# Kernel optimization log

Measured on AMD Instinct MI355X. Metric: run time of the kernel, lower is better.

## Reference

```python
import jax, jax.numpy as jnp
import numpy as np

FS = 20.832e6      # sampling rate [Hz]
FDEMOD = 5.208e6   # demodulation frequency [Hz]
C = 1540.0         # sound speed [m/s]
FNUM = 1.0
MIN_W = 1e-3
EPS = 1e-5         # BatchNorm eps
EVENT = 0
TWO_PI = 2.0 * np.pi


def _cba(x, w, b, g, beta, pad):
    # Conv2d (NCHW) + BatchNorm2d (training-mode batch stats, biased var) + ReLU
    y = jax.lax.conv_general_dilated(x, w, (1, 1), ((0, 0), (pad, pad)),
                                     dimension_numbers=('NCHW', 'OIHW', 'NCHW'))
    y = y + b[None, :, None, None]
    mu = jnp.mean(y, axis=(0, 2, 3), keepdims=True)
    var = jnp.mean((y - mu) ** 2, axis=(0, 2, 3), keepdims=True)
    y = (y - mu) * jax.lax.rsqrt(var + EPS) * g[None, :, None, None] + beta[None, :, None, None]
    return jax.nn.relu(y)


def _forward(idata, qdata, angles, ele_pos, time_zero, grid,
             conv_w1, conv_b1, bn_g1, bn_b1,
             conv_w2, conv_b2, bn_g2, bn_b2,
             conv_w3, conv_b3, bn_g3, bn_b3,
             conv_w4, conv_b4, bn_g4, bn_b4):
    # --- normalization of raw I/Q data ---
    nrm = jnp.max(jnp.sqrt(idata ** 2 + qdata ** 2))
    idat = idata / nrm
    qdat = qdata / nrm
    H, Wd = grid.shape[:2]
    pix = grid.reshape(-1, 3)                               # [P,3]
    E = ele_pos.shape[0]
    ns = idat.shape[-1]
    ang = angles[EVENT]
    # --- delays in samples: plane-wave tx delay + per-element rx focus delay ---
    txdel = (pix[:, 0] * jnp.sin(ang) + pix[:, 2] * jnp.cos(ang)
             + time_zero[EVENT] * C) * (FS / C)             # [P]
    rxdel = jnp.linalg.norm(pix[None, :, :] - ele_pos[:, None, :], axis=-1) * (FS / C)  # [E,P]
    delays = txdel[None, :] + rxdel                         # [E,P]
    # --- 1D linear interp with zero padding ---
    # (grid_sample(bilinear, align_corners=False) on a 1xN image with the
    #  coordinate mapping in the source is exactly sampling at `delays`)
    d0 = jnp.floor(delays)
    frac = delays - d0
    d0i = d0.astype(jnp.int32)

    def gather(sig, idx):  # sig [E,ns], idx [E,P]
        v = jnp.take_along_axis(sig, jnp.clip(idx, 0, ns - 1), axis=1)
        return jnp.where((idx >= 0) & (idx < ns), v, 0.0)

    isig, qsig = idat[EVENT], qdat[EVENT]                   # [E,ns]
    ifoc = gather(isig, d0i) * (1.0 - frac) + gather(isig, d0i + 1) * frac
    qfoc = gather(qsig, d0i) * (1.0 - frac) + gather(qsig, d0i + 1) * frac
    # --- complex demodulation rotation ---
    tshift = delays / FS - pix[None, :, 2] * 2.0 / C
    theta = TWO_PI * FDEMOD * tshift
    ct, st = jnp.cos(theta), jnp.sin(theta)
    ir = ifoc * ct - qfoc * st
    qr = qfoc * ct + ifoc * st
    # [1,H,W,E,2]  (== torch idas/qdas view + squeeze(-2))
    inputData = jnp.transpose(jnp.stack([ir, qr], axis=-1), (1, 0, 2)).reshape(H, Wd, E, 2)[None]
    # --- receive apodization (orthogonal f-number mask), [H,W,E] ---
    v = pix[None, :, :] - ele_pos[:, None, :]
    vx, vz = v[:, :, 0], v[:, :, 2]
    px = pix[None, :, 0]
    # |vz/vx| > fnum written division-free as |vz| > fnum*|vx| (equivalent since vz>0)
    mrx = ((jnp.abs(vz) > FNUM * jnp.abs(vx)) | (jnp.abs(vx) <= MIN_W)
           | ((vx >= MIN_W) & (px <= ele_pos[0, 0]))
           | ((vx <= -MIN_W) & (px >= ele_pos[-1, 0])))
    apod_rx = jnp.transpose(mrx.astype(jnp.float32).reshape(E, H, Wd), (1, 2, 0))
    # --- transmit apodization (plane-wave footprint), [H,W] ---
    x_proj = pix[:, 0] - pix[:, 2] * jnp.tan(ang)
    mtx = (x_proj >= ele_pos[0, 0] * 1.2) & (x_proj <= ele_pos[-1, 0] * 1.2)
    apod_tx = mtx.astype(jnp.float32).reshape(H, Wd)
    inputData = inputData * apod_rx[None, :, :, :, None] * apod_tx[None, :, :, None, None]
    # --- per-element weighting CNN over [1, 2, H*W, E] ---
    x = jnp.transpose(inputData, (0, 4, 3, 1, 2)).reshape(1, 2, E, H * Wd)
    x = jnp.swapaxes(x, 2, 3)                               # [1,2,HW,E]
    x = _cba(x, conv_w1, conv_b1, bn_g1, bn_b1, 32)
    x = _cba(x, conv_w2, conv_b2, bn_g2, bn_b2, 7)
    x = _cba(x, conv_w3, conv_b3, bn_g3, bn_b3, 7)
    x = _cba(x, conv_w4, conv_b4, bn_g4, bn_b4, 1)          # [1,1,HW,E]
    weights = jnp.swapaxes(x[:, 0], 1, 2).reshape(1, E, H, Wd)
    singleW = jnp.sum(weights, axis=1)                      # [1,H,W]
    comp = jnp.mean(inputData * singleW[:, :, :, None, None], axis=-2)  # [1,H,W,2]
    mag = jnp.sqrt(jnp.sum(comp ** 2, axis=-1))
    ydb = 20.0 * jnp.log10(mag + 1e-20)
    y = ydb[0]
    return y - jnp.max(y)


def setup_inputs():
    key = jax.random.key(0)
    ks = jax.random.split(key, 8)
    na, ne, ns = 16, 128, 2048
    H, Wd = 128, 256
    idata = jax.random.normal(ks[0], (na, ne, ns), jnp.float32)
    qdata = jax.random.normal(ks[1], (na, ne, ns), jnp.float32)
    angles = jnp.linspace(-0.1, 0.1, na, dtype=jnp.float32)
    ex = jnp.linspace(-19.05e-3, 19.05e-3, ne, dtype=jnp.float32)
    ele_pos = jnp.stack([ex, jnp.zeros(ne, jnp.float32), jnp.zeros(ne, jnp.float32)], axis=-1)
    time_zero = jnp.zeros((na,), jnp.float32)
    xg = jnp.linspace(-17e-3, 17e-3, H, dtype=jnp.float32)
    zg = jnp.linspace(5e-3, 55e-3, Wd, dtype=jnp.float32)
    gx, gz = jnp.meshgrid(xg, zg, indexing='ij')
    grid = jnp.stack([gx, jnp.zeros_like(gx), gz], axis=-1)

    def conv_init(k, o, i, kh, kw):
        return jax.random.normal(k, (o, i, kh, kw), jnp.float32) * (1.0 / np.sqrt(i * kh * kw))

    return dict(idata=idata, qdata=qdata, angles=angles, ele_pos=ele_pos,
                time_zero=time_zero, grid=grid,
                conv_w1=conv_init(ks[2], 8, 2, 1, 65), conv_b1=jnp.zeros(8, jnp.float32),
                bn_g1=jnp.ones(8, jnp.float32), bn_b1=jnp.zeros(8, jnp.float32),
                conv_w2=conv_init(ks[3], 8, 8, 1, 15), conv_b2=jnp.zeros(8, jnp.float32),
                bn_g2=jnp.ones(8, jnp.float32), bn_b2=jnp.zeros(8, jnp.float32),
                conv_w3=conv_init(ks[4], 8, 8, 1, 15), conv_b3=jnp.zeros(8, jnp.float32),
                bn_g3=jnp.ones(8, jnp.float32), bn_b3=jnp.zeros(8, jnp.float32),
                conv_w4=conv_init(ks[5], 1, 8, 1, 3), conv_b4=jnp.zeros(1, jnp.float32),
                bn_g4=jnp.ones(1, jnp.float32), bn_b4=jnp.zeros(1, jnp.float32))


def reference(idata, qdata, angles, ele_pos, time_zero, grid,
              conv_w1, conv_b1, bn_g1, bn_b1,
              conv_w2, conv_b2, bn_g2, bn_b2,
              conv_w3, conv_b3, bn_g3, bn_b3,
              conv_w4, conv_b4, bn_g4, bn_b4):
    return _forward(idata, qdata, angles, ele_pos, time_zero, grid,
                    conv_w1, conv_b1, bn_g1, bn_b1,
                    conv_w2, conv_b2, bn_g2, bn_b2,
                    conv_w3, conv_b3, bn_g3, bn_b3,
                    conv_w4, conv_b4, bn_g4, bn_b4)
```

## Files before the change

kernel.cpp:

```cpp
#include <hip/hip_runtime.h>
#include <hip/hip_bf16.h>


#define E_    128
#define NPIX  32768
#define NS_   (NPIX * E_)
#define NSAMP 2048

static constexpr double PI_D     = 3.14159265358979323846;
static constexpr double FS_D     = 20832000.0;
static constexpr double FDEMOD_D = 5208000.0;
static constexpr double C_D      = 1540.0;

typedef __attribute__((ext_vector_type(8))) short short8;
typedef __attribute__((ext_vector_type(4))) float f32x4;

union U8 { uint4 u4; unsigned u32[4]; unsigned short us[8]; short8 s8; };

__device__ __forceinline__ unsigned short f2bf(float f) {
  unsigned u = __float_as_uint(f);
  unsigned r = (u + 0x7fffu + ((u >> 16) & 1u)) >> 16;
  return (unsigned short)r;
}
__device__ __forceinline__ unsigned cvt_pk_bf16(float lo, float hi) {
  unsigned r;
  asm("v_cvt_pk_bf16_f32 %0, %1, %2" : "=v"(r) : "v"(lo), "v"(hi));
  return r;
}
__device__ __forceinline__ float bflo(unsigned w) { return __uint_as_float(w << 16); }
__device__ __forceinline__ float bfhi(unsigned w) { return __uint_as_float(w & 0xFFFF0000u); }
__device__ __forceinline__ float bf2f(unsigned short s) {
  return __uint_as_float((unsigned)s << 16);
}

__device__ __forceinline__ float wave_reduce_sum(float v) {
  #pragma unroll
  for (int off = 32; off; off >>= 1) v += __shfl_xor(v, off);
  return v;
}
__device__ __forceinline__ float wave_reduce_max(float v) {
  #pragma unroll
  for (int off = 32; off; off >>= 1) v = fmaxf(v, __shfl_xor(v, off));
  return v;
}

__device__ __forceinline__ uint4 bn_unit(uint4 v, const float* A, const float* B) {
  U8 in; in.u4 = v;
  unsigned ow[4];
  #pragma unroll
  for (int w = 0; w < 4; ++w) {
    const unsigned wd = in.u32[w];
    const float yl = fmaxf(0.f, fmaf(A[2 * w], bflo(wd), B[2 * w]));
    const float yh = fmaxf(0.f, fmaf(A[2 * w + 1], bfhi(wd), B[2 * w + 1]));
    ow[w] = cvt_pk_bf16(yl, yh);
  }
  return make_uint4(ow[0], ow[1], ow[2], ow[3]);
}

__global__ __launch_bounds__(256) void k_init(const float4* __restrict__ id4,
                                              const float4* __restrict__ qd4,
                                              float* __restrict__ pmaxsq) {
  const int idx = blockIdx.x * 256 + threadIdx.x;
  const float4 iv = id4[idx];
  const float4 qv = qd4[idx];
  float m = fmaxf(fmaxf(iv.x * iv.x + qv.x * qv.x, iv.y * iv.y + qv.y * qv.y),
                  fmaxf(iv.z * iv.z + qv.z * qv.z, iv.w * iv.w + qv.w * qv.w));
  m = wave_reduce_max(m);
  __shared__ float sm[4];
  if ((threadIdx.x & 63) == 0) sm[threadIdx.x >> 6] = m;
  __syncthreads();
  if (threadIdx.x == 0)
    pmaxsq[blockIdx.x] = fmaxf(fmaxf(sm[0], sm[1]), fmaxf(sm[2], sm[3]));
}

__global__ __launch_bounds__(256) void k_beamform(
    const float4* __restrict__ id4, const float4* __restrict__ qd4,
    const float* __restrict__ angles, const float* __restrict__ ele_pos,
    const float* __restrict__ time_zero, const float* __restrict__ grid,
    const float* __restrict__ pmaxsq, unsigned* __restrict__ x0t) {
  __shared__ float2 sig[NSAMP];
  __shared__ float smax[4];
  const int e = blockIdx.x & 127;
  const int chunk = blockIdx.x >> 7;

  const float4* irow = id4 + e * (NSAMP / 4);
  const float4* qrow = qd4 + e * (NSAMP / 4);
  #pragma unroll
  for (int k0 = 0; k0 < 2; ++k0) {
    const int k = k0 * 256 + threadIdx.x;
    const float4 iv = irow[k];
    const float4 qv = qrow[k];
    sig[4 * k + 0] = make_float2(iv.x, qv.x);
    sig[4 * k + 1] = make_float2(iv.y, qv.y);
    sig[4 * k + 2] = make_float2(iv.z, qv.z);
    sig[4 * k + 3] = make_float2(iv.w, qv.w);
  }
  float mx = 0.f;
  for (int i = threadIdx.x; i < 4096; i += 256) mx = fmaxf(mx, pmaxsq[i]);
  mx = wave_reduce_max(mx);
  if ((threadIdx.x & 63) == 0) smax[threadIdx.x >> 6] = mx;
  __syncthreads();
  const float inv =
      1.0f / sqrtf(fmaxf(fmaxf(smax[0], smax[1]), fmaxf(smax[2], smax[3])));

  const float ang = angles[0];
  const float tz  = time_zero[0];

  constexpr float SC    = (float)(FS_D / C_D);
  constexpr float TH2R  = (float)(2.0 * FDEMOD_D / C_D);
  constexpr float TWOPI = (float)(2.0 * PI_D);

  const float sa = __sinf(ang);
  const float ca = __cosf(ang);
  const float ta = sa / ca;
  const float ex  = ele_pos[e * 3];
  const float ex0 = ele_pos[0];
  const float exl = ele_pos[127 * 3];

  #pragma unroll
  for (int s = 0; s < 4; ++s) {
    const int p = chunk * 1024 + s * 256 + threadIdx.x;
    const float px = grid[p * 3 + 0];
    const float pz = grid[p * 3 + 2];

    const float txdel = (px * sa + pz * ca + tz * (float)C_D) * SC;
    const float dx = px - ex;
    const float rxdel = sqrtf(dx * dx + pz * pz) * SC;

    const float delays = txdel + rxdel;
    const float d0 = floorf(delays);
    const float frac = delays - d0;
    const int i0 = (int)d0;

    const int c0 = min(max(i0, 0), NSAMP - 1);
    const int c1 = min(max(i0 + 1, 0), NSAMP - 1);
    const float2 s0 = sig[c0];
    const float2 s1 = sig[c1];
    const bool m0 = (i0 >= 0) && (i0 < NSAMP);
    const bool m1 = (i0 + 1 >= 0) && (i0 + 1 < NSAMP);
    const float iv0 = m0 ? s0.x : 0.f;
    const float qv0 = m0 ? s0.y : 0.f;
    const float iv1 = m1 ? s1.x : 0.f;
    const float qv1 = m1 ? s1.y : 0.f;
    const float ifoc = (iv0 * (1.f - frac) + iv1 * frac) * inv;
    const float qfoc = (qv0 * (1.f - frac) + qv1 * frac) * inv;

    const float trev = fmaf(delays, 0.25f, -pz * TH2R);
    const float fr = trev - floorf(trev);
    const float st = __sinf(fr * TWOPI);
    const float ct = __cosf(fr * TWOPI);
    const float ir = ifoc * ct - qfoc * st;
    const float qr = qfoc * ct + ifoc * st;

    const float avx = fabsf(dx);
    const bool mrx = (fabsf(pz) > avx) || (avx <= 0.001f) ||
                     ((dx >= 0.001f) && (px <= ex0)) ||
                     ((dx <= -0.001f) && (px >= exl));
    const float xproj = px - pz * ta;
    const bool mtx = (xproj >= ex0 * 1.2f) && (xproj <= exl * 1.2f);
    const float a = (mrx && mtx) ? 1.f : 0.f;

    x0t[(size_t)e * NPIX + p] = cvt_pk_bf16(ir * a, qr * a);
  }
}

#define CONV1_P 32
#define ROWW    213

__global__ __launch_bounds__(256, 4) void k_conv1(
    const unsigned* __restrict__ x0t, const float* __restrict__ wgt,
    const float* __restrict__ bias, uint2* __restrict__ outp,
    float* __restrict__ partial,
    float* __restrict__ sumI, float* __restrict__ sumQ) {
  __shared__ unsigned tile[CONV1_P * ROWW];
  const int tid = threadIdx.x;
  const int lane = tid & 63;
  const int wv = tid >> 6;
  const int n = lane & 15, kq = lane >> 4;
  const int p0 = blockIdx.x * CONV1_P;

  short8 af2[6];
  #pragma unroll
  for (int m = 0; m < 6; ++m) {
    U8 u;
    #pragma unroll
    for (int j = 0; j < 8; ++j) {
      const int oc = n & 7;
      const int mm = (n < 8) ? m : (m - 1);
      const int tap = mm * 16 + kq * 4 + (j >> 1);
      const int ic = j & 1;
      const float w = (mm >= 0 && tap < 65) ? wgt[(oc * 2 + ic) * 65 + tap] : 0.f;
      u.us[j] = f2bf(w);
    }
    af2[m] = u.s8;
  }
  float bias_r[4];
  #pragma unroll
  for (int r = 0; r < 4; ++r) bias_r[r] = bias[(kq & 1) * 4 + r];

  for (int i = tid; i < CONV1_P * 32; i += 256)
    tile[(i >> 5) * ROWW + (i & 31)] = 0u;
  for (int i = tid; i < CONV1_P * 64; i += 256) {
    const int c = i & 63;
    if (c < ROWW - 160) tile[(i >> 6) * ROWW + 160 + c] = 0u;
  }
  {
    const int lp = tid & 31;
    const int e0 = tid >> 5;
    #pragma unroll
    for (int i = 0; i < 16; ++i) {
      const int e = i * 8 + e0;
      tile[lp * ROWW + 32 + e] = x0t[(size_t)e * NPIX + p0 + lp];
    }
  }
  __syncthreads();

  float sum[4] = {0, 0, 0, 0}, ssq[4] = {0, 0, 0, 0};
  const int sbase = n + kq * 4;

  for (int j8 = 0; j8 < 8; ++j8) {
    const int lpx = wv * 8 + j8;
    const int p = p0 + lpx;
    const unsigned* row = tile + lpx * ROWW;
    uint2* orow = outp + (size_t)p * 256;

    {
      const unsigned v0 = row[32 + lane];
      const unsigned v1 = row[96 + lane];
      float si = bflo(v0) + bflo(v1);
      float sq = bfhi(v0) + bfhi(v1);
      si = wave_reduce_sum(si);
      sq = wave_reduce_sum(sq);
      if (lane == 0) { sumI[p] = si; sumQ[p] = sq; }
    }

    U8 win[12];
    #pragma unroll
    for (int q = 0; q < 12; ++q)
      #pragma unroll
      for (int c = 0; c < 4; ++c) win[q].u32[c] = row[sbase + 16 * q + c];

    #pragma unroll
    for (int pi = 0; pi < 4; ++pi) {
      f32x4 acc = {bias_r[0], bias_r[1], bias_r[2], bias_r[3]};
      #pragma unroll
      for (int m = 0; m < 6; ++m)
        acc = __builtin_amdgcn_mfma_f32_16x16x32_bf16(af2[m], win[2 * pi + m].s8,
                                                      acc, 0, 0, 0);
      const unsigned lo = cvt_pk_bf16(acc[0], acc[1]);
      const unsigned hi = cvt_pk_bf16(acc[2], acc[3]);
      orow[((2 * pi + (kq >> 1)) * 16 + n) * 2 + (kq & 1)] = make_uint2(lo, hi);
      #pragma unroll
      for (int r = 0; r < 4; ++r) { const float v = acc[r]; sum[r] += v; ssq[r] += v * v; }
    }
  }

  #pragma unroll
  for (int off = 1; off <= 8; off <<= 1)
    #pragma unroll
    for (int r = 0; r < 4; ++r) { sum[r] += __shfl_xor(sum[r], off); ssq[r] += __shfl_xor(ssq[r], off); }
  #pragma unroll
  for (int r = 0; r < 4; ++r) { sum[r] += __shfl_xor(sum[r], 32); ssq[r] += __shfl_xor(ssq[r], 32); }
  __shared__ float s_red[4][16];
  if (lane == 0)
    #pragma unroll
    for (int r = 0; r < 4; ++r) { s_red[wv][r] = sum[r]; s_red[wv][8 + r] = ssq[r]; }
  if (lane == 16)
    #pragma unroll
    for (int r = 0; r < 4; ++r) { s_red[wv][4 + r] = sum[r]; s_red[wv][12 + r] = ssq[r]; }
  __syncthreads();
  if (tid < 16)
    partial[blockIdx.x * 16 + tid] =
        s_red[0][tid] + s_red[1][tid] + s_red[2][tid] + s_red[3][tid];
}

__global__ __launch_bounds__(256) void k_conv23(
    const uint4* __restrict__ inp, const float* __restrict__ wgt,
    const float* __restrict__ bias, const float* __restrict__ bnAB,
    uint2* __restrict__ outp, float* __restrict__ partial) {
  __shared__ uint4 s_row[4][144];
  const int tid = threadIdx.x;
  const int lane = tid & 63;
  const int wv = tid >> 6;
  const int gw = blockIdx.x * 4 + wv;
  const int n = lane & 15, kq = lane >> 4;

  float A[8], Bc[8];
  #pragma unroll
  for (int i = 0; i < 8; ++i) { A[i] = bnAB[2 * i]; Bc[i] = bnAB[2 * i + 1]; }

  short8 af[4];
  #pragma unroll
  for (int m = 0; m < 4; ++m) {
    U8 u;
    #pragma unroll
    for (int j = 0; j < 8; ++j) {
      const int tap = m * 4 + kq;
      const float w = (n < 8 && tap < 15) ? wgt[(n * 8 + j) * 15 + tap] : 0.f;
      u.us[j] = f2bf(w);
    }
    af[m] = u.s8;
  }
  float bias_r[4];
  #pragma unroll
  for (int r = 0; r < 4; ++r) {
    const int oo = kq * 4 + r;
    bias_r[r] = (oo < 8) ? bias[oo] : 0.f;
  }

  uint4* lds = s_row[wv];
  if (lane < 7)  lds[lane] = make_uint4(0, 0, 0, 0);
  if (lane >= 7 && lane < 16) lds[128 + lane] = make_uint4(0, 0, 0, 0);

  float sum[4] = {0, 0, 0, 0}, ssq[4] = {0, 0, 0, 0};

  uint4 v0 = inp[(size_t)gw * 128 + lane];
  uint4 v1 = inp[(size_t)gw * 128 + 64 + lane];

  #pragma unroll 1
  for (int it = 0; it < 4; ++it) {
    const int p = gw + it * 8192;
    lds[7 + lane]  = bn_unit(v0, A, Bc);
    lds[71 + lane] = bn_unit(v1, A, Bc);

    if (it < 3) {
      const uint4* ng = inp + (size_t)(p + 8192) * 128;
      v0 = ng[lane];
      v1 = ng[64 + lane];
    }

    uint2* orow = outp + (size_t)p * 256;
    for (int t = 0; t < 8; ++t) {
      f32x4 acc = {bias_r[0], bias_r[1], bias_r[2], bias_r[3]};
      const int base = t * 16 + n + kq;
      #pragma unroll
      for (int m = 0; m < 4; ++m) {
        U8 b;
        b.u4 = lds[base + m * 4];
        acc = __builtin_amdgcn_mfma_f32_16x16x32_bf16(af[m], b.s8, acc, 0, 0, 0);
      }
      if (lane < 32) {
        const unsigned lo = cvt_pk_bf16(acc[0], acc[1]);
        const unsigned hi = cvt_pk_bf16(acc[2], acc[3]);
        orow[(t * 16 + n) * 2 + kq] = make_uint2(lo, hi);
        #pragma unroll
        for (int r = 0; r < 4; ++r) { const float v = acc[r]; sum[r] += v; ssq[r] += v * v; }
      }
    }
  }

  #pragma unroll
  for (int off = 1; off <= 8; off <<= 1)
    #pragma unroll
    for (int r = 0; r < 4; ++r) { sum[r] += __shfl_xor(sum[r], off); ssq[r] += __shfl_xor(ssq[r], off); }
  __shared__ float s_red[4][16];
  if (lane == 0)
    #pragma unroll
    for (int r = 0; r < 4; ++r) { s_red[wv][r] = sum[r]; s_red[wv][8 + r] = ssq[r]; }
  if (lane == 16)
    #pragma unroll
    for (int r = 0; r < 4; ++r) { s_red[wv][4 + r] = sum[r]; s_red[wv][12 + r] = ssq[r]; }
  __syncthreads();
  if (tid < 16)
    partial[blockIdx.x * 16 + tid] =
        s_red[0][tid] + s_red[1][tid] + s_red[2][tid] + s_red[3][tid];
}

__global__ __launch_bounds__(256) void k_conv4(
    const uint4* __restrict__ inp, const float* __restrict__ bnAB,
    const float* __restrict__ w4, const float* __restrict__ b4,
    unsigned short* __restrict__ y4b, float* __restrict__ partial) {
  const int idx = blockIdx.x * 256 + threadIdx.x;
  const int p = idx >> 7, e = idx & 127;

  float A[8], Bc[8];
  #pragma unroll
  for (int i = 0; i < 8; ++i) { A[i] = bnAB[2 * i]; Bc[i] = bnAB[2 * i + 1]; }

  float acc = b4[0];
  const uint4* row = inp + (size_t)p * 128 + e;
  #pragma unroll
  for (int kt = 0; kt < 3; ++kt) {
    const int ee = e + kt - 1;
    if (ee >= 0 && ee < E_) {
      U8 u; u.u4 = row[kt - 1];
      #pragma unroll
      for (int i = 0; i < 8; ++i) {
        const unsigned wd = u.u32[i >> 1];
        const float x = (i & 1) ? bfhi(wd) : bflo(wd);
        const float v = fmaxf(0.f, fmaf(A[i], x, Bc[i]));
        acc = fmaf(w4[i * 3 + kt], v, acc);
      }
    }
  }
  y4b[idx] = f2bf(acc);

  float s = wave_reduce_sum(acc);
  float ss = wave_reduce_sum(acc * acc);
  __shared__ float sm[4][2];
  if ((threadIdx.x & 63) == 0) { sm[threadIdx.x >> 6][0] = s; sm[threadIdx.x >> 6][1] = ss; }
  __syncthreads();
  if (threadIdx.x == 0) {
    partial[blockIdx.x * 2 + 0] = sm[0][0] + sm[1][0] + sm[2][0] + sm[3][0];
    partial[blockIdx.x * 2 + 1] = sm[0][1] + sm[1][1] + sm[2][1] + sm[3][1];
  }
}

__global__ __launch_bounds__(256) void k_stats(const float* __restrict__ partial,
                                               int nblk, int oc,
                                               const float* __restrict__ g,
                                               const float* __restrict__ beta,
                                               float* __restrict__ ssout) {
  const int o = blockIdx.x;
  float s = 0.f, ss = 0.f;
  for (int b = threadIdx.x; b < nblk; b += 256) {
    s  += partial[b * 2 * oc + o];
    ss += partial[b * 2 * oc + oc + o];
  }
  s = wave_reduce_sum(s);
  ss = wave_reduce_sum(ss);
  __shared__ float sm[4][2];
  if ((threadIdx.x & 63) == 0) { sm[threadIdx.x >> 6][0] = s; sm[threadIdx.x >> 6][1] = ss; }
  __syncthreads();
  if (threadIdx.x == 0) {
    s  = sm[0][0] + sm[1][0] + sm[2][0] + sm[3][0];
    ss = sm[0][1] + sm[1][1] + sm[2][1] + sm[3][1];
    const float count = (float)NS_;
    const float mu = s / count;
    const float var = fmaxf(ss / count - mu * mu, 0.f);
    const float Av = g[o] * rsqrtf(var + 1e-5f);
    ssout[2 * o] = Av;
    ssout[2 * o + 1] = beta[o] - mu * Av;
  }
}

__global__ __launch_bounds__(256) void k_final(const float* __restrict__ sumI,
                                               const float* __restrict__ sumQ,
                                               const unsigned short* __restrict__ y4b,
                                               const float* __restrict__ ss4,
                                               float* __restrict__ ydb,
                                               float* __restrict__ pmax) {
  const int w = threadIdx.x >> 6;
  const int lane = threadIdx.x & 63;
  const int p = blockIdx.x * 4 + w;
  const float A = ss4[0], B = ss4[1];
  const size_t base = (size_t)p * E_;

  float sw = fmaxf(0.f, fmaf(A, bf2f(y4b[base + lane]), B)) +
             fmaxf(0.f, fmaf(A, bf2f(y4b[base + lane + 64]), B));
  sw = wave_reduce_sum(sw);

  __shared__ float s_m[4];
  if (lane == 0) {
    const float ci = sw * sumI[p] * (1.f / (float)E_);
    const float cq = sw * sumQ[p] * (1.f / (float)E_);
    const float mag = sqrtf(ci * ci + cq * cq);
    const float v = 20.f * log10f(mag + 1e-20f);
    ydb[p] = v;
    s_m[w] = v;
  }
  __syncthreads();
  if (threadIdx.x == 0)
    pmax[blockIdx.x] = fmaxf(fmaxf(s_m[0], s_m[1]), fmaxf(s_m[2], s_m[3]));
}

__global__ __launch_bounds__(256) void k_sub(const float* __restrict__ ydb,
                                             const float* __restrict__ pmax,
                                             float* __restrict__ out) {
  float m = -3.4e38f;
  for (int i = threadIdx.x; i < NPIX / 4; i += 256) m = fmaxf(m, pmax[i]);
  m = wave_reduce_max(m);
  __shared__ float sm[4];
  if ((threadIdx.x & 63) == 0) sm[threadIdx.x >> 6] = m;
  __syncthreads();
  __shared__ float sgm;
  if (threadIdx.x == 0)
    sgm = fmaxf(fmaxf(sm[0], sm[1]), fmaxf(sm[2], sm[3]));
  __syncthreads();
  const int i = blockIdx.x * 256 + threadIdx.x;
  out[i] = ydb[i] - sgm;
}

static constexpr size_t OFF_A     = 0;
static constexpr size_t OFF_Y4    = 0;
static constexpr size_t OFF_YDB   = 16777216;
static constexpr size_t OFF_PMAX  = 16908288;
static constexpr size_t OFF_BUF1  = 67108864;
static constexpr size_t OFF_SUMI  = 134217728;
static constexpr size_t OFF_SUMQ  = 134348800;
static constexpr size_t OFF_PART  = 134479872;
static constexpr size_t OFF_PMSQ  = 134742016;
static constexpr size_t OFF_SS    = 134758400;

extern "C" void kernel_launch(void* const* d_in, const int* in_sizes, int n_in,
                              void* d_out, int out_size, void* d_ws, size_t ws_size,
                              hipStream_t stream) {
  const float* idata     = (const float*)d_in[0];
  const float* qdata     = (const float*)d_in[1];
  const float* angles    = (const float*)d_in[2];
  const float* ele_pos   = (const float*)d_in[3];
  const float* time_zero = (const float*)d_in[4];
  const float* grid      = (const float*)d_in[5];
  const float* w1 = (const float*)d_in[6];  const float* b1 = (const float*)d_in[7];
  const float* g1 = (const float*)d_in[8];  const float* be1 = (const float*)d_in[9];
  const float* w2 = (const float*)d_in[10]; const float* b2 = (const float*)d_in[11];
  const float* g2 = (const float*)d_in[12]; const float* be2 = (const float*)d_in[13];
  const float* w3 = (const float*)d_in[14]; const float* b3 = (const float*)d_in[15];
  const float* g3 = (const float*)d_in[16]; const float* be3 = (const float*)d_in[17];
  const float* w4 = (const float*)d_in[18]; const float* b4 = (const float*)d_in[19];
  const float* g4 = (const float*)d_in[20]; const float* be4 = (const float*)d_in[21];

  char* ws = (char*)d_ws;
  unsigned*       x0t   = (unsigned*)(ws + OFF_A);
  uint4*          buf2  = (uint4*)(ws + OFF_A);
  unsigned short* y4b   = (unsigned short*)(ws + OFF_Y4);
  float*          ydb   = (float*)(ws + OFF_YDB);
  float*          pmax  = (float*)(ws + OFF_PMAX);
  uint4*          buf1  = (uint4*)(ws + OFF_BUF1);
  float*          sumI  = (float*)(ws + OFF_SUMI);
  float*          sumQ  = (float*)(ws + OFF_SUMQ);
  float*          part  = (float*)(ws + OFF_PART);
  float*          pmsq  = (float*)(ws + OFF_PMSQ);
  float*          ssAB  = (float*)(ws + OFF_SS);

  k_init<<<4096, 256, 0, stream>>>((const float4*)idata, (const float4*)qdata, pmsq);
  k_beamform<<<4096, 256, 0, stream>>>((const float4*)idata, (const float4*)qdata,
                                       angles, ele_pos, time_zero, grid,
                                       pmsq, x0t);

  k_conv1<<<NPIX / CONV1_P, 256, 0, stream>>>(x0t, w1, b1, (uint2*)buf1, part,
                                              sumI, sumQ);
  k_stats<<<8, 256, 0, stream>>>(part, NPIX / CONV1_P, 8, g1, be1, ssAB + 0);

  k_conv23<<<2048, 256, 0, stream>>>(buf1, w2, b2, ssAB + 0, (uint2*)buf2, part);
  k_stats<<<8, 256, 0, stream>>>(part, 2048, 8, g2, be2, ssAB + 16);

  k_conv23<<<2048, 256, 0, stream>>>(buf2, w3, b3, ssAB + 16, (uint2*)buf1, part);
  k_stats<<<8, 256, 0, stream>>>(part, 2048, 8, g3, be3, ssAB + 32);

  k_conv4<<<NS_ / 256, 256, 0, stream>>>(buf1, ssAB + 32, w4, b4, y4b, part);
  k_stats<<<1, 256, 0, stream>>>(part, NS_ / 256, 1, g4, be4, ssAB + 48);

  k_final<<<NPIX / 4, 256, 0, stream>>>(sumI, sumQ, y4b, ssAB + 48, ydb, pmax);
  k_sub<<<NPIX / 256, 256, 0, stream>>>(ydb, pmax, (float*)d_out);
}
```

Measured before the change: 276.3 us.

## Fold BatchNorm stats reduction into consumer kernels and drop k_stats launches

Removes the four small k_stats launches by having each consumer kernel (conv23, conv4, final) redundantly reduce the previous layer's per-block partial sums and compute BN scale/shift at block start. Partial buffers are ping-ponged between two workspace regions so that producer and consumer don't alias. conv4 is also changed to a grid-stride form with 2048 blocks that loop 8 times, so its partial count drops to 2048 and k_final can reduce them cheaply. This saves launch gaps and serialization, but every block now rereads thousands of partials, which adds redundant global reads and a few extra barriers.

```diff
diff --git a/kernel.cpp b/kernel.cpp
--- a/kernel.cpp
+++ b/kernel.cpp
@@ -42,6 +42,39 @@
   #pragma unroll
   for (int off = 32; off; off >>= 1) v = fmaxf(v, __shfl_xor(v, off));
   return v;
+}
+
+__device__ __forceinline__ void stats8(const float* __restrict__ partial,
+                                       int nblk,
+                                       const float* __restrict__ g,
+                                       const float* __restrict__ beta,
+                                       float* __restrict__ A,
+                                       float* __restrict__ Bc) {
+  __shared__ float red[4][16];
+  __shared__ float sums[16];
+  const int tid = threadIdx.x;
+  float acc = 0.f;
+  for (int b = tid >> 4; b < nblk; b += 16)
+    acc += partial[b * 16 + (tid & 15)];
+  acc += __shfl_xor(acc, 16);
+  acc += __shfl_xor(acc, 32);
+  if ((tid & 63) < 16) red[tid >> 6][tid & 15] = acc;
+  __syncthreads();
+  if (tid < 16)
+    sums[tid] = red[0][tid] + red[1][tid] + red[2][tid] + red[3][tid];
+  __syncthreads();
+  if (tid < 8) {
+    const float s = sums[tid], ss = sums[tid + 8];
+    const float count = (float)NS_;
+    const float mu = s / count;
+    const float var = fmaxf(ss / count - mu * mu, 0.f);
+    const float Av = g[tid] * rsqrtf(var + 1e-5f);
+    red[0][tid] = Av;
+    red[1][tid] = beta[tid] - mu * Av;
+  }
+  __syncthreads();
+  #pragma unroll
+  for (int i = 0; i < 8; ++i) { A[i] = red[0][i]; Bc[i] = red[1][i]; }
 }
 
 __device__ __forceinline__ uint4 bn_unit(uint4 v, const float* A, const float* B) {
@@ -276,7 +309,9 @@
 
 __global__ __launch_bounds__(256) void k_conv23(
     const uint4* __restrict__ inp, const float* __restrict__ wgt,
-    const float* __restrict__ bias, const float* __restrict__ bnAB,
+    const float* __restrict__ bias,
+    const float* __restrict__ part_in, int nblk_in,
+    const float* __restrict__ g_in, const float* __restrict__ be_in,
     uint2* __restrict__ outp, float* __restrict__ partial) {
   __shared__ uint4 s_row[4][144];
   const int tid = threadIdx.x;
@@ -285,9 +320,11 @@
   const int gw = blockIdx.x * 4 + wv;
   const int n = lane & 15, kq = lane >> 4;
 
+  uint4 v0 = inp[(size_t)gw * 128 + lane];
+  uint4 v1 = inp[(size_t)gw * 128 + 64 + lane];
+
   float A[8], Bc[8];
-  #pragma unroll
-  for (int i = 0; i < 8; ++i) { A[i] = bnAB[2 * i]; Bc[i] = bnAB[2 * i + 1]; }
+  stats8(part_in, nblk_in, g_in, be_in, A, Bc);
 
   short8 af[4];
   #pragma unroll
@@ -313,9 +350,6 @@
   if (lane >= 7 && lane < 16) lds[128 + lane] = make_uint4(0, 0, 0, 0);
 
   float sum[4] = {0, 0, 0, 0}, ssq[4] = {0, 0, 0, 0};
-
-  uint4 v0 = inp[(size_t)gw * 128 + lane];
-  uint4 v1 = inp[(size_t)gw * 128 + 64 + lane];
 
   #pragma unroll 1
   for (int it = 0; it < 4; ++it) {
@@ -367,83 +401,95 @@
 }
 
 __global__ __launch_bounds__(256) void k_conv4(
-    const uint4* __restrict__ inp, const float* __restrict__ bnAB,
+    const uint4* __restrict__ inp,
+    const float* __restrict__ part_in,
+    const float* __restrict__ g3, const float* __restrict__ be3,
     const float* __restrict__ w4, const float* __restrict__ b4,
     unsigned short* __restrict__ y4b, float* __restrict__ partial) {
-  const int idx = blockIdx.x * 256 + threadIdx.x;
-  const int p = idx >> 7, e = idx & 127;
-
   float A[8], Bc[8];
-  #pragma unroll
-  for (int i = 0; i < 8; ++i) { A[i] = bnAB[2 * i]; Bc[i] = bnAB[2 * i + 1]; }
-
-  float acc = b4[0];
-  const uint4* row = inp + (size_t)p * 128 + e;
-  #pragma unroll
-  for (int kt = 0; kt < 3; ++kt) {
-    const int ee = e + kt - 1;
-    if (ee >= 0 && ee < E_) {
-      U8 u; u.u4 = row[kt - 1];
-      #pragma unroll
-      for (int i = 0; i < 8; ++i) {
-        const unsigned wd = u.u32[i >> 1];
-        const float x = (i & 1) ? bfhi(wd) : bflo(wd);
-        const float v = fmaxf(0.f, fmaf(A[i], x, Bc[i]));
-        acc = fmaf(w4[i * 3 + kt], v, acc);
+  stats8(part_in, 2048, g3, be3, A, Bc);
+
+  const float bb = b4[0];
+  float w4r[24];
+  #pragma unroll
+  for (int i = 0; i < 24; ++i) w4r[i] = w4[i];
+
+  float s = 0.f, ss = 0.f;
+  #pragma unroll 1
+  for (int it = 0; it < 8; ++it) {
+    const int idx = blockIdx.x * 256 + threadIdx.x + it * 524288;
+    const int p = idx >> 7, e = idx & 127;
+    float acc = bb;
+    const uint4* row = inp + (size_t)p * 128 + e;
+    #pragma unroll
+    for (int kt = 0; kt < 3; ++kt) {
+      const int ee = e + kt - 1;
+      if (ee >= 0 && ee < E_) {
+        U8 u; u.u4 = row[kt - 1];
+        #pragma unroll
+        for (int i = 0; i < 8; ++i) {
+          const unsigned wd = u.u32[i >> 1];
+          const float x = (i & 1) ? bfhi(wd) : bflo(wd);
+          const float v = fmaxf(0.f, fmaf(A[i], x, Bc[i]));
+          acc = fmaf(w4r[i * 3 + kt], v, acc);
+        }
       }
     }
-  }
-  y4b[idx] = f2bf(acc);
-
-  float s = wave_reduce_sum(acc);
-  float ss = wave_reduce_sum(acc * acc);
-  __shared__ float sm[4][2];
-  if ((threadIdx.x & 63) == 0) { sm[threadIdx.x >> 6][0] = s; sm[threadIdx.x >> 6][1] = ss; }
-  __syncthreads();
-  if (threadIdx.x == 0) {
-    partial[blockIdx.x * 2 + 0] = sm[0][0] + sm[1][0] + sm[2][0] + sm[3][0];
-    partial[blockIdx.x * 2 + 1] = sm[0][1] + sm[1][1] + sm[2][1] + sm[3][1];
-  }
-}
-
-__global__ __launch_bounds__(256) void k_stats(const float* __restrict__ partial,
-                                               int nblk, int oc,
-                                               const float* __restrict__ g,
-                                               const float* __restrict__ beta,
-                                               float* __restrict__ ssout) {
-  const int o = blockIdx.x;
-  float s = 0.f, ss = 0.f;
-  for (int b = threadIdx.x; b < nblk; b += 256) {
-    s  += partial[b * 2 * oc + o];
-    ss += partial[b * 2 * oc + oc + o];
-  }
+    y4b[idx] = f2bf(acc);
+    s += acc;
+    ss += acc * acc;
+  }
+
   s = wave_reduce_sum(s);
   ss = wave_reduce_sum(ss);
   __shared__ float sm[4][2];
   if ((threadIdx.x & 63) == 0) { sm[threadIdx.x >> 6][0] = s; sm[threadIdx.x >> 6][1] = ss; }
   __syncthreads();
   if (threadIdx.x == 0) {
-    s  = sm[0][0] + sm[1][0] + sm[2][0] + sm[3][0];
-    ss = sm[0][1] + sm[1][1] + sm[2][1] + sm[3][1];
-    const float count = (float)NS_;
-    const float mu = s / count;
-    const float var = fmaxf(ss / count - mu * mu, 0.f);
-    const float Av = g[o] * rsqrtf(var + 1e-5f);
-    ssout[2 * o] = Av;
-    ssout[2 * o + 1] = beta[o] - mu * Av;
+    partial[blockIdx.x * 2 + 0] = sm[0][0] + sm[1][0] + sm[2][0] + sm[3][0];
+    partial[blockIdx.x * 2 + 1] = sm[0][1] + sm[1][1] + sm[2][1] + sm[3][1];
   }
 }
 
 __global__ __launch_bounds__(256) void k_final(const float* __restrict__ sumI,
                                                const float* __restrict__ sumQ,
                                                const unsigned short* __restrict__ y4b,
-                                               const float* __restrict__ ss4,
+                                               const float* __restrict__ part_in,
+                                               const float* __restrict__ g4,
+                                               const float* __restrict__ be4,
                                                float* __restrict__ ydb,
                                                float* __restrict__ pmax) {
+  __shared__ float sAB[2];
+  {
+    const int tid = threadIdx.x;
+    float s = 0.f, ss = 0.f;
+    for (int b = tid; b < 2048; b += 256) {
+      const float2 v = ((const float2*)part_in)[b];
+      s += v.x;
+      ss += v.y;
+    }
+    s = wave_reduce_sum(s);
+    ss = wave_reduce_sum(ss);
+    __shared__ float sm[4][2];
+    if ((tid & 63) == 0) { sm[tid >> 6][0] = s; sm[tid >> 6][1] = ss; }
+    __syncthreads();
+    if (tid == 0) {
+      s  = sm[0][0] + sm[1][0] + sm[2][0] + sm[3][0];
+      ss = sm[0][1] + sm[1][1] + sm[2][1] + sm[3][1];
+      const float count = (float)NS_;
+      const float mu = s / count;
+      const float var = fmaxf(ss / count - mu * mu, 0.f);
+      const float Av = g4[0] * rsqrtf(var + 1e-5f);
+      sAB[0] = Av;
+      sAB[1] = be4[0] - mu * Av;
+    }
+    __syncthreads();
+  }
+  const float A = sAB[0], B = sAB[1];
+
   const int w = threadIdx.x >> 6;
   const int lane = threadIdx.x & 63;
   const int p = blockIdx.x * 4 + w;
-  const float A = ss4[0], B = ss4[1];
   const size_t base = (size_t)p * E_;
 
   float sw = fmaxf(0.f, fmaf(A, bf2f(y4b[base + lane]), B)) +
@@ -488,9 +534,9 @@
 static constexpr size_t OFF_BUF1  = 67108864;
 static constexpr size_t OFF_SUMI  = 134217728;
 static constexpr size_t OFF_SUMQ  = 134348800;
-static constexpr size_t OFF_PART  = 134479872;
+static constexpr size_t OFF_PART0 = 134479872;
+static constexpr size_t OFF_PART1 = 134610944;
 static constexpr size_t OFF_PMSQ  = 134742016;
-static constexpr size_t OFF_SS    = 134758400;
 
 extern "C" void kernel_launch(void* const* d_in, const int* in_sizes, int n_in,
                               void* d_out, int out_size, void* d_ws, size_t ws_size,
@@ -519,28 +565,27 @@
   uint4*          buf1  = (uint4*)(ws + OFF_BUF1);
   float*          sumI  = (float*)(ws + OFF_SUMI);
   float*          sumQ  = (float*)(ws + OFF_SUMQ);
-  float*          part  = (float*)(ws + OFF_PART);
+  float*          part0 = (float*)(ws + OFF_PART0);
+  float*          part1 = (float*)(ws + OFF_PART1);
   float*          pmsq  = (float*)(ws + OFF_PMSQ);
-  float*          ssAB  = (float*)(ws + OFF_SS);
 
   k_init<<<4096, 256, 0, stream>>>((const float4*)idata, (const float4*)qdata, pmsq);
   k_beamform<<<4096, 256, 0, stream>>>((const float4*)idata, (const float4*)qdata,
                                        angles, ele_pos, time_zero, grid,
                                        pmsq, x0t);
 
-  k_conv1<<<NPIX / CONV1_P, 256, 0, stream>>>(x0t, w1, b1, (uint2*)buf1, part,
+  k_conv1<<<NPIX / CONV1_P, 256, 0, stream>>>(x0t, w1, b1, (uint2*)buf1, part0,
                                               sumI, sumQ);
-  k_stats<<<8, 256, 0, stream>>>(part, NPIX / CONV1_P, 8, g1, be1, ssAB + 0);
-
-  k_conv23<<<2048, 256, 0, stream>>>(buf1, w2, b2, ssAB + 0, (uint2*)buf2, part);
-  k_stats<<<8, 256, 0, stream>>>(part, 2048, 8, g2, be2, ssAB + 16);
-
-  k_conv23<<<2048, 256, 0, stream>>>(buf2, w3, b3, ssAB + 16, (uint2*)buf1, part);
-  k_stats<<<8, 256, 0, stream>>>(part, 2048, 8, g3, be3, ssAB + 32);
-
-  k_conv4<<<NS_ / 256, 256, 0, stream>>>(buf1, ssAB + 32, w4, b4, y4b, part);
-  k_stats<<<1, 256, 0, stream>>>(part, NS_ / 256, 1, g4, be4, ssAB + 48);
-
-  k_final<<<NPIX / 4, 256, 0, stream>>>(sumI, sumQ, y4b, ssAB + 48, ydb, pmax);
+
+  k_conv23<<<2048, 256, 0, stream>>>(buf1, w2, b2, part0, NPIX / CONV1_P,
+                                     g1, be1, (uint2*)buf2, part1);
+
+  k_conv23<<<2048, 256, 0, stream>>>(buf2, w3, b3, part1, 2048,
+                                     g2, be2, (uint2*)buf1, part0);
+
+  k_conv4<<<2048, 256, 0, stream>>>(buf1, part0, g3, be3, w4, b4, y4b, part1);
+
+  k_final<<<NPIX / 4, 256, 0, stream>>>(sumI, sumQ, y4b, part1, g4, be4,
+                                        ydb, pmax);
   k_sub<<<NPIX / 256, 256, 0, stream>>>(ydb, pmax, (float*)d_out);
 }
```

Result: slower. 379.2 us (+37.2%).
